# Kernel tuning notes

Measured on AMD Instinct MI355X. Metric: run time of the kernel, lower is better.

The kernel has to match this reference:

```python
import jax, jax.numpy as jnp
import numpy as np

N_NODES = 16384


def gcn_conv(x, edge_index, W, b):
    """GCNConv: out = D^{-1/2} (A + I) D^{-1/2} (x @ W) + b."""
    n = x.shape[0]
    xw = x @ W  # [n, out_dim] -- transform before propagate (PyG order)
    loops = jnp.arange(n)
    src = jnp.concatenate([edge_index[0], loops])
    dst = jnp.concatenate([edge_index[1], loops])
    ones = jnp.ones(src.shape[0], dtype=xw.dtype)
    deg = jax.ops.segment_sum(ones, dst, num_segments=n)  # degree incl. self-loops
    dinv = jnp.where(deg > 0, jax.lax.rsqrt(deg), 0.0)
    norm = dinv[src] * dinv[dst]  # [E + n]
    msg = xw[src] * norm[:, None]  # gather + scale
    out = jax.ops.segment_sum(msg, dst, num_segments=n)  # scatter-add aggregate
    return out + b


def setup_inputs() -> dict:
    key = jax.random.key(0)
    ks = jax.random.split(key, 8)
    N, E, C = N_NODES, 524288, 7
    x = jax.random.normal(ks[0], (N, N), dtype=jnp.float32)
    edge_index = jax.random.randint(ks[1], (2, E), 0, N, dtype=jnp.int64)
    W1 = jax.random.normal(ks[2], (N, 50), dtype=jnp.float32) * (1.0 / np.sqrt(N))
    b1 = jnp.zeros((50,), dtype=jnp.float32)
    W2 = jax.random.normal(ks[3], (50, 2), dtype=jnp.float32) * (1.0 / np.sqrt(50))
    b2 = jnp.zeros((2,), dtype=jnp.float32)
    Wc = jax.random.normal(ks[4], (2, C), dtype=jnp.float32) * (1.0 / np.sqrt(2))
    bc = jnp.zeros((C,), dtype=jnp.float32)
    return {"x": x, "edge_index": edge_index, "W1": W1, "b1": b1,
            "W2": W2, "b2": b2, "Wc": Wc, "bc": bc}


def reference(x, edge_index, W1, b1, W2, b2, Wc, bc):
    h = jnp.tanh(gcn_conv(x, edge_index, W1, b1))   # [N, 50]
    h = jnp.tanh(gcn_conv(h, edge_index, W2, b2))   # [N, 2]
    out = h @ Wc + bc                               # [N, num_classes]
    return (out, h)
```

## Files before the change

### kernel.cpp

```cpp
#include <hip/hip_runtime.h>

typedef float  f32x4  __attribute__((ext_vector_type(4)));
typedef __bf16 bf16x8 __attribute__((ext_vector_type(8)));

#define N_NODES 16384
#define K_DIM   16384
#define H1_DIM  50
#define H1_PAD  64
#define CAP     160
#define OUT_OFF (N_NODES * 7)

typedef const __attribute__((address_space(1))) unsigned int* gas_ptr;
typedef __attribute__((address_space(3))) unsigned int* las_ptr;
__device__ __forceinline__ void gload_lds16(const void* g, void* l) {
  __builtin_amdgcn_global_load_lds((gas_ptr)g, (las_ptr)l, 16, 0, 0);
}

__global__ __launch_bounds__(256) void k_pre(const float* __restrict__ W1, __bf16* __restrict__ WT,
                                             const int* __restrict__ src, const int* __restrict__ dst,
                                             int E, int* cnt, int* bucket) {
  int t = threadIdx.x;
  if (blockIdx.x < 256) {
    __shared__ __bf16 lds[64][80];
    int k0 = blockIdx.x * 64;
    int rq = t >> 6, c = t & 63;
    for (int r = 0; r < 16; ++r) {
      int row = rq * 16 + r;
      __bf16 v = (__bf16)0.f;
      if (c < H1_DIM) v = (__bf16)W1[(size_t)(k0 + row) * H1_DIM + c];
      lds[c][row] = v;
    }
    __syncthreads();
    int cw = t >> 2, kq = (t & 3) * 16;
    __bf16* dp = WT + (size_t)cw * K_DIM + k0 + kq;
    *(bf16x8*)dp       = *(const bf16x8*)&lds[cw][kq];
    *((bf16x8*)dp + 1) = *(const bf16x8*)&lds[cw][kq + 8];
  } else {
    int e = (blockIdx.x - 256) * 256 + t;
    if (e < E) {
      int d = dst[e];
      int pos = atomicAdd(&cnt[d], 1);
      if (pos < CAP) bucket[(size_t)d * CAP + pos] = src[e];
    }
  }
}

__global__ __launch_bounds__(256) void k_dinv(const int* __restrict__ cnt, float* __restrict__ dinv) {
  int i = blockIdx.x * 256 + threadIdx.x;
  dinv[i] = rsqrtf((float)(cnt[i] + 1));
}

__global__ __launch_bounds__(256) void k_gemm1(const float* __restrict__ x,
                                               const __bf16* __restrict__ WT,
                                               const float* __restrict__ dinv,
                                               float* __restrict__ xw) {
  __shared__ float  As[64 * 64];
  __shared__ __bf16 Bs[64 * 64];
  int tid = threadIdx.x;
  int w = tid >> 6, l = tid & 63;
  int l15 = l & 15, l7 = l & 7, g2 = l >> 4;
  int row0 = blockIdx.x * 64;
  int kbase = blockIdx.y * 4096;

  int a_row = w * 4 + (l >> 4);
  int b_col = w * 8 + (l >> 3);
  int m_row = w * 16 + l15;

  f32x4 acc0 = {0,0,0,0}, acc1 = {0,0,0,0}, acc2 = {0,0,0,0}, acc3 = {0,0,0,0};

  for (int ks = 0; ks < 64; ++ks) {
    int kk = kbase + ks * 64;
#pragma unroll
    for (int c = 0; c < 4; ++c) {
      int r = c * 16 + a_row;
      const float* gp = x + (size_t)(row0 + r) * K_DIM + kk + ((l15 ^ (r & 15)) << 2);
      gload_lds16(gp, &As[c * 1024 + w * 256]);
    }
#pragma unroll
    for (int c = 0; c < 2; ++c) {
      int col = c * 32 + b_col;
      const __bf16* gp = WT + (size_t)col * K_DIM + kk + ((l7 ^ (col & 7)) << 3);
      gload_lds16(gp, &Bs[c * 2048 + w * 512]);
    }
    __syncthreads();
#pragma unroll
    for (int s = 0; s < 2; ++s) {
      int c0 = s * 8 + g2 * 2;
      f32x4 a0 = *(const f32x4*)&As[m_row * 64 + (((c0    ) ^ l15) << 2)];
      f32x4 a1 = *(const f32x4*)&As[m_row * 64 + (((c0 + 1) ^ l15) << 2)];
      bf16x8 af;
      af[0] = (__bf16)a0[0]; af[1] = (__bf16)a0[1]; af[2] = (__bf16)a0[2]; af[3] = (__bf16)a0[3];
      af[4] = (__bf16)a1[0]; af[5] = (__bf16)a1[1]; af[6] = (__bf16)a1[2]; af[7] = (__bf16)a1[3];
      int cb = (s * 4 + g2) ^ l7;
      bf16x8 b0 = *(const bf16x8*)&Bs[(     l15) * 64 + (cb << 3)];
      bf16x8 b1 = *(const bf16x8*)&Bs[(16 + l15) * 64 + (cb << 3)];
      bf16x8 b2 = *(const bf16x8*)&Bs[(32 + l15) * 64 + (cb << 3)];
      bf16x8 b3 = *(const bf16x8*)&Bs[(48 + l15) * 64 + (cb << 3)];
      acc0 = __builtin_amdgcn_mfma_f32_16x16x32_bf16(af, b0, acc0, 0, 0, 0);
      acc1 = __builtin_amdgcn_mfma_f32_16x16x32_bf16(af, b1, acc1, 0, 0, 0);
      acc2 = __builtin_amdgcn_mfma_f32_16x16x32_bf16(af, b2, acc2, 0, 0, 0);
      acc3 = __builtin_amdgcn_mfma_f32_16x16x32_bf16(af, b3, acc3, 0, 0, 0);
    }
    __syncthreads();
  }

  int crow = row0 + w * 16 + g2 * 4;
#pragma unroll
  for (int j = 0; j < 4; ++j) {
    float dv = dinv[crow + j];
    size_t rb = (size_t)(crow + j) * H1_PAD + l15;
    atomicAdd(&xw[rb],      acc0[j] * dv);
    atomicAdd(&xw[rb + 16], acc1[j] * dv);
    atomicAdd(&xw[rb + 32], acc2[j] * dv);
    atomicAdd(&xw[rb + 48], acc3[j] * dv);
  }
}

__global__ __launch_bounds__(256) void k_agg1(const float* __restrict__ xw,
                                              const int* __restrict__ cnt,
                                              const int* __restrict__ bucket,
                                              const float* __restrict__ dinv,
                                              const float* __restrict__ b1,
                                              const float* __restrict__ W2,
                                              float* __restrict__ xw2s) {
  int tid = threadIdx.x;
  int nid = blockIdx.x * 4 + (tid >> 6);
  int j = tid & 63;
  float acc = xw[(size_t)nid * H1_PAD + j];
  int cn = cnt[nid];
  if (cn > CAP) cn = CAP;
  const int* bp = bucket + (size_t)nid * CAP;
  int p = 0;
  for (; p + 3 < cn; p += 4) {
    int s0 = bp[p], s1 = bp[p + 1], s2 = bp[p + 2], s3 = bp[p + 3];
    acc += xw[(size_t)s0 * H1_PAD + j];
    acc += xw[(size_t)s1 * H1_PAD + j];
    acc += xw[(size_t)s2 * H1_PAD + j];
    acc += xw[(size_t)s3 * H1_PAD + j];
  }
  for (; p < cn; ++p) acc += xw[(size_t)bp[p] * H1_PAD + j];

  float dv = dinv[nid];
  float bj = (j < H1_DIM) ? b1[j] : 0.f;
  float h = tanhf(dv * acc + bj);
  float w0 = (j < H1_DIM) ? W2[j * 2]     : 0.f;
  float w1 = (j < H1_DIM) ? W2[j * 2 + 1] : 0.f;
  float a0 = h * w0, a1 = h * w1;
#pragma unroll
  for (int off = 32; off >= 1; off >>= 1) {
    a0 += __shfl_xor(a0, off);
    a1 += __shfl_xor(a1, off);
  }
  if (j == 0) {
    xw2s[nid * 2]     = a0 * dv;
    xw2s[nid * 2 + 1] = a1 * dv;
  }
}

__global__ __launch_bounds__(256) void k_final(const float* __restrict__ xw2s,
                                               const int* __restrict__ cnt,
                                               const int* __restrict__ bucket,
                                               const float* __restrict__ dinv,
                                               const float* __restrict__ b2,
                                               const float* __restrict__ Wc,
                                               const float* __restrict__ bc,
                                               float* __restrict__ dout) {
  int tid = threadIdx.x;
  int g = tid >> 4, r = tid & 15;
  int nid = blockIdx.x * 16 + g;
  int cn = cnt[nid];
  if (cn > CAP) cn = CAP;
  const int* bp = bucket + (size_t)nid * CAP;
  float a0 = 0.f, a1 = 0.f;
  for (int p = r; p < cn; p += 16) {
    int sc = bp[p];
    a0 += xw2s[sc * 2];
    a1 += xw2s[sc * 2 + 1];
  }
#pragma unroll
  for (int off = 8; off >= 1; off >>= 1) {
    a0 += __shfl_xor(a0, off, 16);
    a1 += __shfl_xor(a1, off, 16);
  }
  if (r == 0) {
    a0 += xw2s[nid * 2];
    a1 += xw2s[nid * 2 + 1];
    float dv = dinv[nid];
    float h0  = tanhf(dv * a0 + b2[0]);
    float h1v = tanhf(dv * a1 + b2[1]);
#pragma unroll
    for (int j = 0; j < 7; ++j)
      dout[nid * 7 + j] = h0 * Wc[j] + h1v * Wc[7 + j] + bc[j];
    dout[OUT_OFF + nid * 2]     = h0;
    dout[OUT_OFF + nid * 2 + 1] = h1v;
  }
}

extern "C" void kernel_launch(void* const* d_in, const int* in_sizes, int n_in,
                              void* d_out, int out_size, void* d_ws, size_t ws_size,
                              hipStream_t stream) {
  const float* x  = (const float*)d_in[0];
  const int*   ei = (const int*)d_in[1];
  const float* W1 = (const float*)d_in[2];
  const float* b1 = (const float*)d_in[3];
  const float* W2 = (const float*)d_in[4];
  const float* b2 = (const float*)d_in[5];
  const float* Wc = (const float*)d_in[6];
  const float* bc = (const float*)d_in[7];
  float* dout = (float*)d_out;
  const int E = in_sizes[1] / 2;
  const int* esrc = ei;
  const int* edst = ei + E;

  char* ws = (char*)d_ws;
  float*  xw      = (float*)(ws + 0x0000000);
  __bf16* WT      = (__bf16*)(ws + 0x0400000);
  int*    cnt     = (int*)(ws + 0x0600000);
  float*  dinv    = (float*)(ws + 0x0610000);
  int*    bucket  = (int*)(ws + 0x0620000);
  float*  xw2s    = (float*)(ws + 0x1100000);

  hipMemsetAsync(cnt, 0, N_NODES * sizeof(int), stream);
  hipMemsetAsync(xw, 0, N_NODES * H1_PAD * sizeof(float), stream);
  k_pre<<<256 + (E + 255) / 256, 256, 0, stream>>>(W1, WT, esrc, edst, E, cnt, bucket);
  k_dinv<<<N_NODES / 256, 256, 0, stream>>>(cnt, dinv);
  k_gemm1<<<dim3(256, 4), 256, 0, stream>>>(x, WT, dinv, xw);
  k_agg1<<<N_NODES / 4, 256, 0, stream>>>(xw, cnt, bucket, dinv, b1, W2, xw2s);
  k_final<<<N_NODES / 16, 256, 0, stream>>>(xw2s, cnt, bucket, dinv, b2, Wc, bc, dout);
}
```

Baseline: 277.3 us.

## Halve GEMM k-tile, double split-K grid, and inline dinv computation

Shrinks the GEMM LDS tile from 64 to 32 along K and doubles the split-K factor to 8, with precomputed global pointers and new swizzles. The aim is more resident blocks per CU (launch_bounds 256,8) and more parallelism to saturate HBM bandwidth on the 1 GB fp32 x read. The separate dinv kernel is removed and rsqrt(cnt+1) is computed inline wherever it is needed, saving one launch. The cost is twice as many atomicAdds into xw and more barriers per byte loaded.

```diff
diff --git a/kernel.cpp b/kernel.cpp
--- a/kernel.cpp
+++ b/kernel.cpp
@@ -45,69 +45,61 @@
   }
 }
 
-__global__ __launch_bounds__(256) void k_dinv(const int* __restrict__ cnt, float* __restrict__ dinv) {
-  int i = blockIdx.x * 256 + threadIdx.x;
-  dinv[i] = rsqrtf((float)(cnt[i] + 1));
-}
-
-__global__ __launch_bounds__(256) void k_gemm1(const float* __restrict__ x,
-                                               const __bf16* __restrict__ WT,
-                                               const float* __restrict__ dinv,
-                                               float* __restrict__ xw) {
-  __shared__ float  As[64 * 64];
-  __shared__ __bf16 Bs[64 * 64];
+__global__ __launch_bounds__(256, 8) void k_gemm1(const float* __restrict__ x,
+                                                  const __bf16* __restrict__ WT,
+                                                  const int* __restrict__ cnt,
+                                                  float* __restrict__ xw) {
+  __shared__ float  As[64 * 32];
+  __shared__ __bf16 Bs[64 * 32];
   int tid = threadIdx.x;
   int w = tid >> 6, l = tid & 63;
-  int l15 = l & 15, l7 = l & 7, g2 = l >> 4;
+  int l15 = l & 15, g2 = l >> 4;
   int row0 = blockIdx.x * 64;
-  int kbase = blockIdx.y * 4096;
-
-  int a_row = w * 4 + (l >> 4);
-  int b_col = w * 8 + (l >> 3);
+  int kbase = blockIdx.y * 2048;
+
+  int sa_row = w * 8 + (l >> 3);
+  int sa_chk = l & 7;
+  int sb_col = w * 16 + (l >> 2);
+  int sb_chk = l & 3;
+
+  const float*  ga0 = x + (size_t)(row0 + sa_row) * K_DIM + kbase + ((sa_chk ^ (sa_row & 7)) << 2);
+  const float*  ga1 = ga0 + (size_t)32 * K_DIM;
+  const __bf16* gb  = WT + (size_t)sb_col * K_DIM + kbase + ((sb_chk ^ ((sb_col >> 1) & 3)) << 3);
+
   int m_row = w * 16 + l15;
+  int akey = l15 & 7;
+  int bkey = (l15 >> 1) & 3;
 
   f32x4 acc0 = {0,0,0,0}, acc1 = {0,0,0,0}, acc2 = {0,0,0,0}, acc3 = {0,0,0,0};
 
   for (int ks = 0; ks < 64; ++ks) {
-    int kk = kbase + ks * 64;
-#pragma unroll
-    for (int c = 0; c < 4; ++c) {
-      int r = c * 16 + a_row;
-      const float* gp = x + (size_t)(row0 + r) * K_DIM + kk + ((l15 ^ (r & 15)) << 2);
-      gload_lds16(gp, &As[c * 1024 + w * 256]);
-    }
-#pragma unroll
-    for (int c = 0; c < 2; ++c) {
-      int col = c * 32 + b_col;
-      const __bf16* gp = WT + (size_t)col * K_DIM + kk + ((l7 ^ (col & 7)) << 3);
-      gload_lds16(gp, &Bs[c * 2048 + w * 512]);
-    }
+    int kk = ks * 32;
+    gload_lds16(ga0 + kk, &As[w * 256]);
+    gload_lds16(ga1 + kk, &As[1024 + w * 256]);
+    gload_lds16(gb  + kk, &Bs[w * 512]);
     __syncthreads();
-#pragma unroll
-    for (int s = 0; s < 2; ++s) {
-      int c0 = s * 8 + g2 * 2;
-      f32x4 a0 = *(const f32x4*)&As[m_row * 64 + (((c0    ) ^ l15) << 2)];
-      f32x4 a1 = *(const f32x4*)&As[m_row * 64 + (((c0 + 1) ^ l15) << 2)];
-      bf16x8 af;
-      af[0] = (__bf16)a0[0]; af[1] = (__bf16)a0[1]; af[2] = (__bf16)a0[2]; af[3] = (__bf16)a0[3];
-      af[4] = (__bf16)a1[0]; af[5] = (__bf16)a1[1]; af[6] = (__bf16)a1[2]; af[7] = (__bf16)a1[3];
-      int cb = (s * 4 + g2) ^ l7;
-      bf16x8 b0 = *(const bf16x8*)&Bs[(     l15) * 64 + (cb << 3)];
-      bf16x8 b1 = *(const bf16x8*)&Bs[(16 + l15) * 64 + (cb << 3)];
-      bf16x8 b2 = *(const bf16x8*)&Bs[(32 + l15) * 64 + (cb << 3)];
-      bf16x8 b3 = *(const bf16x8*)&Bs[(48 + l15) * 64 + (cb << 3)];
-      acc0 = __builtin_amdgcn_mfma_f32_16x16x32_bf16(af, b0, acc0, 0, 0, 0);
-      acc1 = __builtin_amdgcn_mfma_f32_16x16x32_bf16(af, b1, acc1, 0, 0, 0);
-      acc2 = __builtin_amdgcn_mfma_f32_16x16x32_bf16(af, b2, acc2, 0, 0, 0);
-      acc3 = __builtin_amdgcn_mfma_f32_16x16x32_bf16(af, b3, acc3, 0, 0, 0);
-    }
+    int s0 = (g2 * 2) ^ akey, s1 = (g2 * 2 + 1) ^ akey;
+    f32x4 a0 = *(const f32x4*)&As[m_row * 32 + s0 * 4];
+    f32x4 a1 = *(const f32x4*)&As[m_row * 32 + s1 * 4];
+    bf16x8 af;
+    af[0] = (__bf16)a0[0]; af[1] = (__bf16)a0[1]; af[2] = (__bf16)a0[2]; af[3] = (__bf16)a0[3];
+    af[4] = (__bf16)a1[0]; af[5] = (__bf16)a1[1]; af[6] = (__bf16)a1[2]; af[7] = (__bf16)a1[3];
+    int sb = (g2 ^ bkey) * 8;
+    bf16x8 b0 = *(const bf16x8*)&Bs[(     l15) * 32 + sb];
+    bf16x8 b1 = *(const bf16x8*)&Bs[(16 + l15) * 32 + sb];
+    bf16x8 b2 = *(const bf16x8*)&Bs[(32 + l15) * 32 + sb];
+    bf16x8 b3 = *(const bf16x8*)&Bs[(48 + l15) * 32 + sb];
+    acc0 = __builtin_amdgcn_mfma_f32_16x16x32_bf16(af, b0, acc0, 0, 0, 0);
+    acc1 = __builtin_amdgcn_mfma_f32_16x16x32_bf16(af, b1, acc1, 0, 0, 0);
+    acc2 = __builtin_amdgcn_mfma_f32_16x16x32_bf16(af, b2, acc2, 0, 0, 0);
+    acc3 = __builtin_amdgcn_mfma_f32_16x16x32_bf16(af, b3, acc3, 0, 0, 0);
     __syncthreads();
   }
 
   int crow = row0 + w * 16 + g2 * 4;
 #pragma unroll
   for (int j = 0; j < 4; ++j) {
-    float dv = dinv[crow + j];
+    float dv = rsqrtf((float)(cnt[crow + j] + 1));
     size_t rb = (size_t)(crow + j) * H1_PAD + l15;
     atomicAdd(&xw[rb],      acc0[j] * dv);
     atomicAdd(&xw[rb + 16], acc1[j] * dv);
@@ -119,7 +111,6 @@
 __global__ __launch_bounds__(256) void k_agg1(const float* __restrict__ xw,
                                               const int* __restrict__ cnt,
                                               const int* __restrict__ bucket,
-                                              const float* __restrict__ dinv,
                                               const float* __restrict__ b1,
                                               const float* __restrict__ W2,
                                               float* __restrict__ xw2s) {
@@ -127,8 +118,8 @@
   int nid = blockIdx.x * 4 + (tid >> 6);
   int j = tid & 63;
   float acc = xw[(size_t)nid * H1_PAD + j];
-  int cn = cnt[nid];
-  if (cn > CAP) cn = CAP;
+  int cn0 = cnt[nid];
+  int cn = cn0 > CAP ? CAP : cn0;
   const int* bp = bucket + (size_t)nid * CAP;
   int p = 0;
   for (; p + 3 < cn; p += 4) {
@@ -140,7 +131,7 @@
   }
   for (; p < cn; ++p) acc += xw[(size_t)bp[p] * H1_PAD + j];
 
-  float dv = dinv[nid];
+  float dv = rsqrtf((float)(cn0 + 1));
   float bj = (j < H1_DIM) ? b1[j] : 0.f;
   float h = tanhf(dv * acc + bj);
   float w0 = (j < H1_DIM) ? W2[j * 2]     : 0.f;
@@ -160,7 +151,6 @@
 __global__ __launch_bounds__(256) void k_final(const float* __restrict__ xw2s,
                                                const int* __restrict__ cnt,
                                                const int* __restrict__ bucket,
-                                               const float* __restrict__ dinv,
                                                const float* __restrict__ b2,
                                                const float* __restrict__ Wc,
                                                const float* __restrict__ bc,
@@ -168,8 +158,8 @@
   int tid = threadIdx.x;
   int g = tid >> 4, r = tid & 15;
   int nid = blockIdx.x * 16 + g;
-  int cn = cnt[nid];
-  if (cn > CAP) cn = CAP;
+  int cn0 = cnt[nid];
+  int cn = cn0 > CAP ? CAP : cn0;
   const int* bp = bucket + (size_t)nid * CAP;
   float a0 = 0.f, a1 = 0.f;
   for (int p = r; p < cn; p += 16) {
@@ -185,7 +175,7 @@
   if (r == 0) {
     a0 += xw2s[nid * 2];
     a1 += xw2s[nid * 2 + 1];
-    float dv = dinv[nid];
+    float dv = rsqrtf((float)(cn0 + 1));
     float h0  = tanhf(dv * a0 + b2[0]);
     float h1v = tanhf(dv * a1 + b2[1]);
 #pragma unroll
@@ -216,15 +206,13 @@
   float*  xw      = (float*)(ws + 0x0000000);
   __bf16* WT      = (__bf16*)(ws + 0x0400000);
   int*    cnt     = (int*)(ws + 0x0600000);
-  float*  dinv    = (float*)(ws + 0x0610000);
   int*    bucket  = (int*)(ws + 0x0620000);
   float*  xw2s    = (float*)(ws + 0x1100000);
 
   hipMemsetAsync(cnt, 0, N_NODES * sizeof(int), stream);
   hipMemsetAsync(xw, 0, N_NODES * H1_PAD * sizeof(float), stream);
   k_pre<<<256 + (E + 255) / 256, 256, 0, stream>>>(W1, WT, esrc, edst, E, cnt, bucket);
-  k_dinv<<<N_NODES / 256, 256, 0, stream>>>(cnt, dinv);
-  k_gemm1<<<dim3(256, 4), 256, 0, stream>>>(x, WT, dinv, xw);
-  k_agg1<<<N_NODES / 4, 256, 0, stream>>>(xw, cnt, bucket, dinv, b1, W2, xw2s);
-  k_final<<<N_NODES / 16, 256, 0, stream>>>(xw2s, cnt, bucket, dinv, b2, Wc, bc, dout);
-}
+  k_gemm1<<<dim3(256, 8), 256, 0, stream>>>(x, WT, cnt, xw);
+  k_agg1<<<N_NODES / 4, 256, 0, stream>>>(xw, cnt, bucket, b1, W2, xw2s);
+  k_final<<<N_NODES / 16, 256, 0, stream>>>(xw2s, cnt, bucket, b2, Wc, bc, dout);
+}
```

Result: slower. 287.4 us (+3.6%).
